# Optimization experiments

Hardware: AMD Instinct MI355X
Metric: run time of the kernel (lower is better)

Reference implementation:

```python
import jax, jax.numpy as jnp
import numpy as np

B, H, W = 8, 256, 256
C = 32          # out_channels / lifted width
CK = 4          # raw k-field channels
M1, M2 = 12, 12  # retained Fourier modes


def _dense_init(key, cin, cout):
    kw, _ = jax.random.split(key)
    w = jax.random.normal(kw, (cin, cout), jnp.float32) / np.float32(np.sqrt(cin))
    b = jnp.zeros((cout,), jnp.float32)
    return w, b


def setup_inputs() -> dict:
    key = jax.random.key(0)
    ks = jax.random.split(key, 16)
    d = {}
    d["x"] = jax.random.normal(ks[0], (B, H, W, C), jnp.float32)
    d["k"] = jax.random.normal(ks[1], (B, H, W, CK), jnp.float32)
    # Project L: Dense(CK->2C), Dense(2C->C)
    d["L_w1"], d["L_b1"] = _dense_init(ks[2], CK, 2 * C)
    d["L_w2"], d["L_b2"] = _dense_init(ks[3], 2 * C, C)
    # Project G
    d["G_w1"], d["G_b1"] = _dense_init(ks[4], CK, 2 * C)
    d["G_w2"], d["G_b2"] = _dense_init(ks[5], 2 * C, C)
    # plain Dense layers
    d["u_w"], d["u_b"] = _dense_init(ks[6], C, C)
    d["Wu_w"], d["Wu_b"] = _dense_init(ks[7], C, C)
    d["Hu_w"], d["Hu_b"] = _dense_init(ks[8], C, C)
    d["Ms_w"], d["Ms_b"] = _dense_init(ks[9], CK, C)
    d["out_w"], d["out_b"] = _dense_init(ks[10], C, C)
    # spectral kernels, init scale = 1/(C_in*C_out)
    scale = np.float32(1.0 / (C * C))
    d["k1r"] = scale * jax.random.normal(ks[11], (C, C, M1, M2), jnp.float32)
    d["k1i"] = scale * jax.random.normal(ks[12], (C, C, M1, M2), jnp.float32)
    d["k2r"] = scale * jax.random.normal(ks[13], (C, C, M1, M2), jnp.float32)
    d["k2i"] = scale * jax.random.normal(ks[14], (C, C, M1, M2), jnp.float32)
    return d


def _project(v, w1, b1, w2, b2):
    return jax.nn.gelu(v @ w1 + b1) @ w2 + b2


def _spectral_conv(v, k1r, k1i, k2r, k2i):
    # v: [B,H,W,C] -> rfft over (H,W); x_ft: [B,H,W//2+1,C] complex
    v_ft = jnp.fft.rfftn(v, axes=(1, 2))
    s1 = jnp.einsum('bijc,coij->bijo', v_ft[:, :M1, :M2, :], k1r + 1j * k1i)
    s2 = jnp.einsum('bijc,coij->bijo', v_ft[:, -M1:, :M2, :], k2r + 1j * k2i)
    out_ft = jnp.zeros_like(v_ft)
    out_ft = out_ft.at[:, :M1, :M2, :].set(s1)
    out_ft = out_ft.at[:, -M1:, :M2, :].set(s2)
    return jnp.fft.irfftn(out_ft, axes=(1, 2))


def reference(x, k,
              L_w1, L_b1, L_w2, L_b2,
              G_w1, G_b1, G_w2, G_b2,
              u_w, u_b, Wu_w, Wu_b, Hu_w, Hu_b, Ms_w, Ms_b,
              out_w, out_b,
              k1r, k1i, k2r, k2i):
    L = _project(k, L_w1, L_b1, L_w2, L_b2)   # [B,H,W,C]
    G = _project(k, G_w1, G_b1, G_w2, G_b2)   # [B,H,W,C]
    u = x @ u_w + u_b
    Wu = u @ Wu_w + Wu_b
    Hu = u @ Hu_w + Hu_b
    Ms = k @ Ms_w + Ms_b
    Fv = _spectral_conv(L * u + Ms, k1r, k1i, k2r, k2i)
    born = Wu - G * (Hu - Fv)
    return jax.nn.gelu(born @ out_w + out_b)
```

## Files before the change

### kernel.cpp

```cpp
#include <hip/hip_runtime.h>
#include <hip/hip_bf16.h>
#include <math.h>

#define BB 8
#define NMODE 24

typedef __attribute__((ext_vector_type(8))) short bf16x8;
typedef __attribute__((ext_vector_type(4))) short bf16x4;
typedef __attribute__((ext_vector_type(4))) float f32x4;

#define MFMA32(a,b,c) __builtin_amdgcn_mfma_f32_16x16x32_bf16(a,b,c,0,0,0)

#if __has_builtin(__builtin_amdgcn_mfma_f32_16x16x16bf16_1k)
#define MFMA16(a,b,c) __builtin_amdgcn_mfma_f32_16x16x16bf16_1k(a,b,c,0,0,0)
#else
static __device__ __forceinline__ f32x4 MFMA16(bf16x4 a, bf16x4 b, f32x4 c){
    f32x4 d;
    asm("v_mfma_f32_16x16x16_bf16 %0, %1, %2, %3" : "=v"(d) : "v"(a), "v"(b), "v"(c));
    return d;
}
#endif

__device__ __forceinline__ unsigned pk2(float lo, float hi){
    __hip_bfloat162 h = __float22bfloat162_rn(make_float2(lo, hi));
    unsigned u; __builtin_memcpy(&u, &h, 4);
    return u;
}
__device__ __forceinline__ short f2b(float f){
    unsigned u = pk2(f, f);
    return (short)u;
}
__device__ __forceinline__ float b2f(short s){
    unsigned u = ((unsigned)(unsigned short)s) << 16;
    return __builtin_bit_cast(float, u);
}
__device__ __forceinline__ bf16x4 cvt4(f32x4 v){
    uint2 t; t.x = pk2(v[0], v[1]); t.y = pk2(v[2], v[3]);
    return __builtin_bit_cast(bf16x4, t);
}
__device__ __forceinline__ bf16x8 cvt8(float4 a, float4 b){
    uint4 t; t.x = pk2(a.x, a.y); t.y = pk2(a.z, a.w);
    t.z = pk2(b.x, b.y); t.w = pk2(b.z, b.w);
    return __builtin_bit_cast(bf16x8, t);
}
__device__ __forceinline__ float gelu_f(float v) {
    float v2  = v * v;
    float arg = v * fmaf(0.10294294f, v2, 2.30220795f);
    float s   = __builtin_amdgcn_exp2f(arg);
    float rc  = __builtin_amdgcn_rcpf(1.0f + s);
    return v - v * rc;
}

__global__ __launch_bounds__(256) void kern0(
    const float* __restrict__ Lw1, const float* __restrict__ Lb1, const float* __restrict__ Lw2,
    const float* __restrict__ Gw1, const float* __restrict__ Gb1, const float* __restrict__ Gw2,
    const float* __restrict__ uw,
    const float* __restrict__ Wuw, const float* __restrict__ Huw,
    const float* __restrict__ Msw, const float* __restrict__ Msb,
    const float* __restrict__ ow,  const float* __restrict__ ob,
    const float* __restrict__ Wub,
    const float* __restrict__ k1r, const float* __restrict__ k1i,
    const float* __restrict__ k2r, const float* __restrict__ k2i,
    short* __restrict__ G1a, short* __restrict__ L1a,
    short* __restrict__ G2T, short* __restrict__ L2T,
    short* __restrict__ WuT, short* __restrict__ HuT,
    short* __restrict__ owT, short* __restrict__ uwT, short* __restrict__ MsA,
    short* __restrict__ basisW, short* __restrict__ basis2P,
    short* __restrict__ basisH1, short* __restrict__ basisH3,
    short* __restrict__ Kp, float* __restrict__ obP)
{
    const int bid = blockIdx.x, t = threadIdx.x;
    const float tp = 6.28318530717958648f/256.f;
    if (bid == 0){
        for (int idx=t; idx<1024; idx+=256){
            int o = idx>>5, c = idx&31;
            WuT[o*32+c] = f2b(Wuw[c*32+o]);
        }
    } else if (bid == 1){
        for (int idx=t; idx<1024; idx+=256){
            int o = idx>>5, c = idx&31;
            HuT[o*32+c] = f2b(Huw[c*32+o]);
        }
    } else if (bid == 2){
        for (int idx=t; idx<1024; idx+=256){
            int hd = idx>>4, k2 = idx&15;
            G1a[idx] = f2b(k2<4 ? Gw1[k2*64+hd] : (k2==4 ? Gb1[hd] : 0.f));
            L1a[idx] = f2b(k2<4 ? Lw1[k2*64+hd] : (k2==4 ? Lb1[hd] : 0.f));
        }
    } else if (bid == 3){
        for (int idx=t; idx<2048; idx+=256){ int o=idx>>6, m=idx&63; G2T[idx]=f2b(Gw2[m*32+o]); }
    } else if (bid == 4){
        for (int idx=t; idx<2048; idx+=256){ int o=idx>>6, m=idx&63; L2T[idx]=f2b(Lw2[m*32+o]); }
    } else if (bid == 5){
        for (int idx=t; idx<1024; idx+=256){
            int o=idx>>5, c=idx&31;
            owT[idx]=f2b(ow[c*32+o]);
            uwT[idx]=f2b(uw[c*32+o]);
        }
    } else if (bid == 6){
        for (int idx=t; idx<512; idx+=256){
            int o=idx>>4, k2=idx&15;
            MsA[idx]=f2b(k2<4 ? Msw[k2*32+o] : (k2==4 ? Msb[o] : 0.f));
        }
        if (t < 32){
            float s = ob[t];
            for (int c=0;c<32;c++) s += Wub[c]*ow[c*32+t];
            obP[t] = s;
        }
    } else if (bid < 15){
        int base=(bid-7)*1024;
        for (int i=t; i<1024; i+=256){
            int idx=base+i; int m=idx>>8, w=idx&255;
            float v=0.f;
            if (m<12)       v = cosf(tp*(float)((m*w)&255));
            else if (m<24)  v = sinf(tp*(float)(((m-12)*w)&255));
            basisW[idx]=f2b(v);
        }
    } else if (bid < 23){
        int base=(bid-15)*1024;
        for (int i=t; i<1024; i+=256){
            int idx=base+i; int w=idx>>5, k=idx&31;
            float v=0.f;
            if (k<24){ int m=k>>1; float a=tp*(float)((m*w)&255); v=(k&1)? -sinf(a):cosf(a); }
            basis2P[idx]=f2b(v);
        }
    } else if (bid < 27){
        int base=(bid-23)*3072;
        for (int i=t; i<3072; i+=256){
            int idx=base+i; int m = idx>>8, h = idx&255;
            int mm = m % 24;
            int ia = (mm<12) ? mm : 232+mm;
            float a = tp*(float)((ia*h)&255);
            basisH1[idx] = f2b(m<24 ? cosf(a) : sinf(a));
        }
    } else if (bid < 35){
        int base=(bid-27)*2048;
        for (int i=t; i<2048; i+=256){
            int idx=base+i; int h = idx>>6, k = idx&63;
            float v = 0.f;
            if (k < 48){
                int mm = k % 24;
                int ia = (mm<12) ? mm : 232+mm;
                float a = tp*(float)((ia*h)&255);
                v = (k<24) ? cosf(a) : sinf(a);
            }
            basisH3[idx] = f2b(v);
        }
    } else {
        int base=(bid-35)*8192;
        for (int i=t; i<8192; i+=256){
            int pid = base + i;
            int o = pid & 31, c = (pid>>5) & 31;
            int rest = pid >> 10;
            int ii = rest % 24, jj = rest / 24;
            int iis = (ii<12) ? ii : ii-12;
            const float* wr = (ii<12) ? k1r : k2r;
            const float* wi = (ii<12) ? k1i : k2i;
            size_t widx = ((size_t)(c*32 + o)*12 + iis)*12 + jj;
            float sc = (jj==0 ? 1.f : 2.f) / 65536.f;
            Kp[2*pid]   = f2b(wr[widx] * sc);
            Kp[2*pid+1] = f2b(wi[widx] * sc);
        }
    }
}


__global__ __launch_bounds__(256, 3) void kernAG(
    const float* __restrict__ x, const float* __restrict__ kk,
    const float* __restrict__ Lb2, const float* __restrict__ ubv,
    const float* __restrict__ Gb2,
    const short* __restrict__ L1a, const short* __restrict__ L2T,
    const short* __restrict__ G1a, const short* __restrict__ G2T,
    const short* __restrict__ uwT, const short* __restrict__ MsA,
    const short* __restrict__ basisW, float* __restrict__ A1,
    float* __restrict__ outw)
{
    __shared__ short vT[32*264];
    const int tid = threadIdx.x, l = tid&63, wv = tid>>6;
    const int q = l>>4, r = l&15;
    const f32x4 z4 = {0.f,0.f,0.f,0.f};

    if (blockIdx.x >= (unsigned)(BB*256)){
        const int bh = blockIdx.x - BB*256;
        short* ug = (short*)outw + (size_t)bh*16384;

        bf16x4 ga[4], g2f[2][4];
        #pragma unroll
        for (int mt=0; mt<4; mt++) ga[mt] = *(const bf16x4*)(G1a + (r+16*mt)*16 + 4*q);
        #pragma unroll
        for (int mt=0; mt<2; mt++)
            #pragma unroll
            for (int ks=0; ks<4; ks++)
                g2f[mt][ks] = *(const bf16x4*)(G2T + (r+16*mt)*64 + 16*ks + 4*q);
        f32x4 gb2v[2];
        #pragma unroll
        for (int mt=0; mt<2; mt++) gb2v[mt] = *(const f32x4*)(Gb2 + 16*mt + 4*q);

        bf16x4 kB[4];
        #pragma unroll
        for (int nt=0; nt<4; nt++){
            const int p = wv*64 + nt*16 + r;
            bf16x4 t = {0,0,0,0};
            if (q==0){
                float4 k4 = *(const float4*)(kk + ((size_t)bh*256 + p)*4);
                uint2 pkk; pkk.x = pk2(k4.x, k4.y); pkk.y = pk2(k4.z, k4.w);
                t = __builtin_bit_cast(bf16x4, pkk);
            } else if (q==1){ t[0] = (short)0x3F80; }
            kB[nt] = t;
        }

        bf16x4 hidG[4][4];
        #pragma unroll
        for (int nt=0; nt<4; nt++)
            #pragma unroll
            for (int mt=0; mt<4; mt++){
                f32x4 acc = MFMA16(ga[mt], kB[nt], z4);
                f32x4 g;
                #pragma unroll
                for (int i=0;i<4;i++) g[i]=gelu_f(acc[i]);
                hidG[nt][mt] = cvt4(g);
            }

        #pragma unroll
        for (int nt=0; nt<4; nt++){
            #pragma unroll
            for (int mt=0; mt<2; mt++){
                f32x4 aG  = MFMA16(g2f[mt][0], hidG[nt][0], gb2v[mt]);
                f32x4 aG2 = MFMA16(g2f[mt][1], hidG[nt][1], z4);
                aG  = MFMA16(g2f[mt][2], hidG[nt][2], aG);
                aG2 = MFMA16(g2f[mt][3], hidG[nt][3], aG2);
                f32x4 gs;
                #pragma unroll
                for (int rg=0; rg<4; rg++) gs[rg] = aG[rg] + aG2[rg];
                *(bf16x4*)(ug + (8 + nt*2+mt)*1024 + tid*4) = cvt4(gs);
            }
        }
        return;
    }

    const int bh = blockIdx.x, b = bh>>8, h = bh&255;

    bf16x4 la[4], ma[2], l2f[2][4];
    bf16x8 ua8[2];
    #pragma unroll
    for (int mt=0; mt<4; mt++) la[mt] = *(const bf16x4*)(L1a + (r+16*mt)*16 + 4*q);
    #pragma unroll
    for (int mt=0; mt<2; mt++){
        ma[mt]  = *(const bf16x4*)(MsA + (r+16*mt)*16 + 4*q);
        ua8[mt] = *(const bf16x8*)(uwT + (r+16*mt)*32 + 8*q);
        #pragma unroll
        for (int ks=0; ks<4; ks++)
            l2f[mt][ks] = *(const bf16x4*)(L2T + (r+16*mt)*64 + 16*ks + 4*q);
    }
    f32x4 lb2v[2], ubv4[2];
    #pragma unroll
    for (int mt=0; mt<2; mt++){
        lb2v[mt] = *(const f32x4*)(Lb2 + 16*mt + 4*q);
        ubv4[mt] = *(const f32x4*)(ubv + 16*mt + 4*q);
    }

    #pragma unroll
    for (int nt=0; nt<4; nt++){
        const int p = wv*64 + nt*16 + r;
        const float* xp = x + ((size_t)bh*256 + p)*32 + 8*q;
        float4 x0 = *(const float4*)xp;
        float4 x1 = *(const float4*)(xp + 4);
        bf16x8 xB8 = cvt8(x0, x1);
        bf16x4 kB = {0,0,0,0};
        if (q==0){
            float4 k4 = *(const float4*)(kk + ((size_t)bh*256 + p)*4);
            uint2 pkk; pkk.x = pk2(k4.x, k4.y); pkk.y = pk2(k4.z, k4.w);
            kB = __builtin_bit_cast(bf16x4, pkk);
        } else if (q==1){ kB[0] = (short)0x3F80; }

        bf16x4 hidL[4];
        #pragma unroll
        for (int mt=0; mt<4; mt++){
            f32x4 accL = MFMA16(la[mt], kB, z4);
            f32x4 gl;
            #pragma unroll
            for (int i=0;i<4;i++) gl[i]=gelu_f(accL[i]);
            hidL[mt] = cvt4(gl);
        }
        #pragma unroll
        for (int mt=0; mt<2; mt++){
            f32x4 aU = MFMA32(ua8[mt], xB8, ubv4[mt]);
            f32x4 aM = MFMA16(ma[mt], kB, z4);
            f32x4 aL  = MFMA16(l2f[mt][0], hidL[0], lb2v[mt]);
            f32x4 aL2 = MFMA16(l2f[mt][1], hidL[1], z4);
            aL  = MFMA16(l2f[mt][2], hidL[2], aL);
            aL2 = MFMA16(l2f[mt][3], hidL[3], aL2);
            f32x4 vv;
            #pragma unroll
            for (int rg=0; rg<4; rg++) vv[rg] = (aL[rg]+aL2[rg]) * aU[rg] + aM[rg];
            bf16x4 vb = cvt4(vv);
            #pragma unroll
            for (int rg=0; rg<4; rg++)
                vT[(16*mt + 4*q + rg)*264 + p] = vb[rg];
        }
    }
    __syncthreads();

    const int mt2 = wv>>1, nt2 = wv&1;
    f32x4 accD = z4;
    #pragma unroll
    for (int ks=0; ks<8; ks++){
        bf16x8 av = *(const bf16x8*)(basisW + (r+16*mt2)*256 + 32*ks + 8*q);
        bf16x8 bv = *(const bf16x8*)(&vT[(r+16*nt2)*264 + 32*ks + 8*q]);
        accD = MFMA32(av, bv, accD);
    }
    #pragma unroll
    for (int rg=0; rg<4; rg++){
        int mode = 16*mt2 + 4*q + rg;
        int ch = r + 16*nt2;
        if (mode < 12)
            A1[((size_t)(b*12+mode)*256 + h)*64 + ch*2] = accD[rg];
        else if (mode < 24)
            A1[((size_t)(b*12+mode-12)*256 + h)*64 + ch*2 + 1] = -accD[rg];
    }
}

__global__ __launch_bounds__(512) void kernC1(
    const float* __restrict__ A1, const short* __restrict__ basisH1,
    const short* __restrict__ Kp, short* __restrict__ SBg)
{
    __shared__ short AT[64*264];
    __shared__ float C1L[48*66];
    const int bj = blockIdx.x;
    const int j  = bj % 12;
    const int tid = threadIdx.x, l = tid&63;
    const int w = tid>>6;
    const int q = l>>4, r = l&15;
    const f32x4 z4 = {0.f,0.f,0.f,0.f};

    {
        const float* Ag = A1 + (size_t)bj*16384;
        for (int i = tid; i < 4096; i += 512){
            float4 v = *(const float4*)(Ag + i*4);
            int hh = (i*4) >> 6;
            int cc = (i*4) & 63;
            AT[(cc+0)*264 + hh] = f2b(v.x);
            AT[(cc+1)*264 + hh] = f2b(v.y);
            AT[(cc+2)*264 + hh] = f2b(v.z);
            AT[(cc+3)*264 + hh] = f2b(v.w);
        }
    }
    __syncthreads();

    {
        const int nt  = w & 3;
        const int nmt = (w < 4) ? 2 : 1;
        const int mt0 = (w < 4) ? 0 : 2;
        f32x4 acc[2] = {z4, z4};
        #pragma unroll
        for (int ks=0; ks<8; ks++){
            bf16x8 bv = *(const bf16x8*)(AT + (nt*16 + r)*264 + ks*32 + q*8);
            #pragma unroll
            for (int mi=0; mi<2; mi++){
                if (mi < nmt){
                    bf16x8 av = *(const bf16x8*)(basisH1 + (r + 16*(mt0+mi))*256 + ks*32 + q*8);
                    acc[mi] = MFMA32(av, bv, acc[mi]);
                }
            }
        }
        #pragma unroll
        for (int mi=0; mi<2; mi++){
            if (mi < nmt){
                #pragma unroll
                for (int rg=0; rg<4; rg++)
                    C1L[(16*(mt0+mi) + 4*q + rg)*66 + 16*nt + r] = acc[mi][rg];
            }
        }
    }
    __syncthreads();

    {
        const int o = tid & 31, g = tid >> 5;
        short* SB = SBg + (size_t)bj*4096;
        #pragma unroll
        for (int half=0; half<2; half++){
            int i = g + 16*half;
            if (i < 24){
                float Sre=0.f, Sim=0.f;
                const short* kp = Kp + ((size_t)(j*24 + i)*32)*64 + 2*o;
                #pragma unroll 4
                for (int c=0; c<32; c++){
                    float vr = C1L[i*66 + 2*c]     + C1L[(24+i)*66 + 2*c+1];
                    float vi = C1L[i*66 + 2*c + 1] - C1L[(24+i)*66 + 2*c];
                    short2 kv = *(const short2*)(kp + c*64);
                    float kr = b2f(kv.x), ki = b2f(kv.y);
                    Sre += vr*kr - vi*ki;
                    Sim += vr*ki + vi*kr;
                }
                SB[o*64 + i]           = f2b(Sre);
                SB[o*64 + 24 + i]      = f2b(-Sim);
                SB[2048 + o*64 + i]    = f2b(Sim);
                SB[2048 + o*64 + 24+i] = f2b(Sre);
            }
        }
        int o2 = (tid >> 4) & 31, kz = 48 + (tid & 15);
        SB[o2*64 + kz] = 0;
        SB[2048 + o2*64 + kz] = 0;
    }
}

__global__ __launch_bounds__(256) void kernC2(
    const short* __restrict__ basisH3, const short* __restrict__ SBg,
    const float* __restrict__ Hub, short* __restrict__ Tp)
{
    __shared__ __align__(16) short Tt[16*1024];
    const int bid = blockIdx.x;
    const int b = bid >> 4, ht = bid & 15;
    const int tid = threadIdx.x, l = tid&63, w = tid>>6;
    const int q = l>>4, r = l&15;
    const f32x4 z4 = {0.f,0.f,0.f,0.f};

    for (int idx = tid; idx < 512; idx += 256){
        int hh = idx >> 5, o = idx & 31;
        #pragma unroll
        for (int kkz=0; kkz<8; kkz++) Tt[(hh*32+o)*32 + 24 + kkz] = 0;
    }

    bf16x8 af[2];
    #pragma unroll
    for (int ks=0; ks<2; ks++)
        af[ks] = *(const bf16x8*)(basisH3 + (ht*16 + r)*64 + ks*32 + q*8);

    #pragma unroll
    for (int jj=0; jj<3; jj++){
        int j = w*3 + jj;
        const short* SB = SBg + (size_t)(b*12 + j)*4096;
        #pragma unroll
        for (int nt=0; nt<2; nt++){
            f32x4 aRe = z4, aIm = z4;
            #pragma unroll
            for (int ks=0; ks<2; ks++){
                bf16x8 b1 = *(const bf16x8*)(SB + (16*nt + r)*64 + ks*32 + q*8);
                bf16x8 b2 = *(const bf16x8*)(SB + 2048 + (16*nt + r)*64 + ks*32 + q*8);
                aRe = MFMA32(af[ks], b1, aRe);
                aIm = MFMA32(af[ks], b2, aIm);
            }
            if (j == 0){
                float hb = Hub[16*nt + r];
                #pragma unroll
                for (int rg=0; rg<4; rg++) aRe[rg] -= hb;
            }
            #pragma unroll
            for (int rg=0; rg<4; rg++){
                int hl = 4*q + rg, o = 16*nt + r;
                *(unsigned*)&Tt[(hl*32 + o)*32 + 2*j] = pk2(aRe[rg], aIm[rg]);
            }
        }
    }
    __syncthreads();

    short* dst = Tp + (size_t)(b*256 + ht*16)*1024;
    #pragma unroll
    for (int it=0; it<8; it++){
        int off = (tid + it*256)*8;
        *(int4*)(dst + off) = *(const int4*)&Tt[off];
    }
}

__global__ __launch_bounds__(256, 3) void kernD(
    const float* __restrict__ x, const float* __restrict__ ubv,
    const float* __restrict__ obP,
    const short* __restrict__ uwT,
    const short* __restrict__ WuT, const short* __restrict__ HuT,
    const short* __restrict__ owT, const short* __restrict__ basis2P,
    const short* __restrict__ Tp, float* out)
{
    const int bh = blockIdx.x;
    const int tid = threadIdx.x, l = tid&63, wv = tid>>6;
    const int q = l>>4, r = l&15;
    const f32x4 z4 = {0.f,0.f,0.f,0.f};
    const short* ug = (const short*)out + (size_t)bh*16384;

    bf16x4 Gf[4][2];
    bf16x8 bb8[4];
    float4 x0[4], x1[4];
    #pragma unroll
    for (int nt=0; nt<4; nt++){
        const int p = wv*64 + nt*16 + r;
        #pragma unroll
        for (int ks=0; ks<2; ks++)
            Gf[nt][ks] = *(const bf16x4*)(ug + (8 + nt*2+ks)*1024 + tid*4);
        bb8[nt] = *(const bf16x8*)(basis2P + p*32 + 8*q);
        const float* xp = x + ((size_t)bh*256 + p)*32 + 8*q;
        x0[nt] = *(const float4*)xp;
        x1[nt] = *(const float4*)(xp + 4);
    }
    bf16x8 tp8[2], ua8[2];
    bf16x4 wuf[2][2], huf[2][2], owf[2][2];
    f32x4 obv2[2], ubv4[2];
    #pragma unroll
    for (int mt=0; mt<2; mt++){
        tp8[mt] = *(const bf16x8*)(Tp + (size_t)bh*1024 + (r+16*mt)*32 + 8*q);
        ua8[mt] = *(const bf16x8*)(uwT + (r+16*mt)*32 + 8*q);
        #pragma unroll
        for (int ks=0; ks<2; ks++){
            wuf[mt][ks] = *(const bf16x4*)(WuT + (r+16*mt)*32 + 16*ks + 4*q);
            huf[mt][ks] = *(const bf16x4*)(HuT + (r+16*mt)*32 + 16*ks + 4*q);
            owf[mt][ks] = *(const bf16x4*)(owT + (r+16*mt)*32 + 16*ks + 4*q);
        }
        obv2[mt] = *(const f32x4*)(obP + 16*mt + 4*q);
        ubv4[mt] = *(const f32x4*)(ubv + 16*mt + 4*q);
    }
    __syncthreads();

    #pragma unroll
    for (int nt=0; nt<4; nt++){
        const int p = wv*64 + nt*16 + r;

        bf16x8 xB8 = cvt8(x0[nt], x1[nt]);
        bf16x4 uB[2];
        #pragma unroll
        for (int mt=0; mt<2; mt++)
            uB[mt] = cvt4(MFMA32(ua8[mt], xB8, ubv4[mt]));

        bf16x4 bornB[2];
        #pragma unroll
        for (int mt=0; mt<2; mt++){
            f32x4 aFv = MFMA32(tp8[mt], bb8[nt], z4);
            f32x4 aHu = MFMA16(huf[mt][0], uB[0], z4);
            aHu = MFMA16(huf[mt][1], uB[1], aHu);
            f32x4 aW  = MFMA16(wuf[mt][0], uB[0], z4);
            aW  = MFMA16(wuf[mt][1], uB[1], aW);
            f32x4 brn;
            #pragma unroll
            for (int rg=0; rg<4; rg++)
                brn[rg] = aW[rg] - b2f(Gf[nt][mt][rg]) * (aHu[rg] - aFv[rg]);
            bornB[mt] = cvt4(brn);
        }
        #pragma unroll
        for (int mt=0; mt<2; mt++){
            f32x4 aO = MFMA16(owf[mt][0], bornB[0], obv2[mt]);
            aO = MFMA16(owf[mt][1], bornB[1], aO);
            float4 res;
            res.x = gelu_f(aO[0]);
            res.y = gelu_f(aO[1]);
            res.z = gelu_f(aO[2]);
            res.w = gelu_f(aO[3]);
            *(float4*)(out + ((size_t)bh*256 + p)*32 + 16*mt + 4*q) = res;
        }
    }
}

extern "C" void kernel_launch(void* const* d_in, const int* in_sizes, int n_in,
                              void* d_out, int out_size, void* d_ws, size_t ws_size,
                              hipStream_t stream)
{
    const float* x   = (const float*)d_in[0];
    const float* kk  = (const float*)d_in[1];
    const float* Lw1 = (const float*)d_in[2];
    const float* Lb1 = (const float*)d_in[3];
    const float* Lw2 = (const float*)d_in[4];
    const float* Lb2 = (const float*)d_in[5];
    const float* Gw1 = (const float*)d_in[6];
    const float* Gb1 = (const float*)d_in[7];
    const float* Gw2 = (const float*)d_in[8];
    const float* Gb2 = (const float*)d_in[9];
    const float* uw  = (const float*)d_in[10];
    const float* ub  = (const float*)d_in[11];
    const float* Wuw = (const float*)d_in[12];
    const float* Wub = (const float*)d_in[13];
    const float* Huw = (const float*)d_in[14];
    const float* Hub = (const float*)d_in[15];
    const float* Msw = (const float*)d_in[16];
    const float* Msb = (const float*)d_in[17];
    const float* ow  = (const float*)d_in[18];
    const float* ob  = (const float*)d_in[19];
    const float* k1r = (const float*)d_in[20];
    const float* k1i = (const float*)d_in[21];
    const float* k2r = (const float*)d_in[22];
    const float* k2i = (const float*)d_in[23];

    float* A1 = (float*)d_ws;
    short* Tp = (short*)(A1 + 1572864);
    short* tab = Tp + 2097152;
    short* G1a  = tab;
    short* L1a  = G1a + 1024;
    short* G2T  = L1a + 1024;
    short* L2T  = G2T + 2048;
    short* WuT  = L2T + 2048;
    short* HuT  = WuT + 1024;
    short* owT  = HuT + 1024;
    short* uwT  = owT + 1024;
    short* MsA  = uwT + 1024;
    short* basisW  = MsA + 512;
    short* basis2P = basisW + 8192;
    short* basisH1 = basis2P + 8192;
    short* basisH3 = basisH1 + 12288;
    short* Kp   = basisH3 + 16384;
    short* SBg  = Kp + 589824;
    float* obP  = (float*)(SBg + 393216);

    float* outp = (float*)d_out;

    kern0<<<71, 256, 0, stream>>>(Lw1, Lb1, Lw2, Gw1, Gb1, Gw2, uw,
                                  Wuw, Huw, Msw, Msb, ow, ob, Wub,
                                  k1r, k1i, k2r, k2i,
                                  G1a, L1a, G2T, L2T, WuT, HuT, owT, uwT, MsA,
                                  basisW, basis2P, basisH1, basisH3, Kp, obP);
    kernAG<<<BB*256*2, 256, 0, stream>>>(x, kk, Lb2, ub, Gb2,
                                         L1a, L2T, G1a, G2T, uwT, MsA, basisW,
                                         A1, outp);
    kernC1<<<BB*12, 512, 0, stream>>>(A1, basisH1, Kp, SBg);
    kernC2<<<BB*16, 256, 0, stream>>>(basisH3, SBg, Hub, Tp);
    kernD<<<BB*256, 256, 0, stream>>>(x, ub, obP, uwT, WuT, HuT, owT,
                                      basis2P, Tp, outp);
}
```

Measured before the change: 124.5 us.

## Stash u in bf16 from kernAG and reuse in kernD instead of recomputing

kernAG now writes the lifted u activation as bf16 into the scratch area of the output buffer, next to the already stored G. kernD reads that u back instead of reloading the fp32 x input and recomputing u with MFMA, so it reads half as many bytes per pixel and drops the uwT/ubv operands. Launch bounds are raised (kernAG 8, kernD 6) to allow more waves per CU. The risk is more global writes in kernAG and register spills under the tighter launch bounds.

```diff
diff --git a/kernel.cpp b/kernel.cpp
--- a/kernel.cpp
+++ b/kernel.cpp
@@ -165,7 +165,7 @@
 }
 
 
-__global__ __launch_bounds__(256, 3) void kernAG(
+__global__ __launch_bounds__(256, 8) void kernAG(
     const float* __restrict__ x, const float* __restrict__ kk,
     const float* __restrict__ Lb2, const float* __restrict__ ubv,
     const float* __restrict__ Gb2,
@@ -239,6 +239,7 @@
     }
 
     const int bh = blockIdx.x, b = bh>>8, h = bh&255;
+    short* ug = (short*)outw + (size_t)bh*16384;
 
     bf16x4 la[4], ma[2], l2f[2][4];
     bf16x8 ua8[2];
@@ -285,6 +286,7 @@
         #pragma unroll
         for (int mt=0; mt<2; mt++){
             f32x4 aU = MFMA32(ua8[mt], xB8, ubv4[mt]);
+            *(bf16x4*)(ug + (nt*2+mt)*1024 + tid*4) = cvt4(aU);
             f32x4 aM = MFMA16(ma[mt], kB, z4);
             f32x4 aL  = MFMA16(l2f[mt][0], hidL[0], lb2v[mt]);
             f32x4 aL2 = MFMA16(l2f[mt][1], hidL[1], z4);
@@ -462,10 +464,8 @@
     }
 }
 
-__global__ __launch_bounds__(256, 3) void kernD(
-    const float* __restrict__ x, const float* __restrict__ ubv,
+__global__ __launch_bounds__(256, 6) void kernD(
     const float* __restrict__ obP,
-    const short* __restrict__ uwT,
     const short* __restrict__ WuT, const short* __restrict__ HuT,
     const short* __restrict__ owT, const short* __restrict__ basis2P,
     const short* __restrict__ Tp, float* out)
@@ -476,27 +476,24 @@
     const f32x4 z4 = {0.f,0.f,0.f,0.f};
     const short* ug = (const short*)out + (size_t)bh*16384;
 
-    bf16x4 Gf[4][2];
+    bf16x4 uB[4][2], Gf[4][2];
     bf16x8 bb8[4];
-    float4 x0[4], x1[4];
     #pragma unroll
     for (int nt=0; nt<4; nt++){
         const int p = wv*64 + nt*16 + r;
         #pragma unroll
-        for (int ks=0; ks<2; ks++)
+        for (int ks=0; ks<2; ks++){
+            uB[nt][ks] = *(const bf16x4*)(ug + (nt*2+ks)*1024 + tid*4);
             Gf[nt][ks] = *(const bf16x4*)(ug + (8 + nt*2+ks)*1024 + tid*4);
+        }
         bb8[nt] = *(const bf16x8*)(basis2P + p*32 + 8*q);
-        const float* xp = x + ((size_t)bh*256 + p)*32 + 8*q;
-        x0[nt] = *(const float4*)xp;
-        x1[nt] = *(const float4*)(xp + 4);
-    }
-    bf16x8 tp8[2], ua8[2];
+    }
+    bf16x8 tp8[2];
     bf16x4 wuf[2][2], huf[2][2], owf[2][2];
-    f32x4 obv2[2], ubv4[2];
+    f32x4 obv2[2];
     #pragma unroll
     for (int mt=0; mt<2; mt++){
         tp8[mt] = *(const bf16x8*)(Tp + (size_t)bh*1024 + (r+16*mt)*32 + 8*q);
-        ua8[mt] = *(const bf16x8*)(uwT + (r+16*mt)*32 + 8*q);
         #pragma unroll
         for (int ks=0; ks<2; ks++){
             wuf[mt][ks] = *(const bf16x4*)(WuT + (r+16*mt)*32 + 16*ks + 4*q);
@@ -504,28 +501,20 @@
             owf[mt][ks] = *(const bf16x4*)(owT + (r+16*mt)*32 + 16*ks + 4*q);
         }
         obv2[mt] = *(const f32x4*)(obP + 16*mt + 4*q);
-        ubv4[mt] = *(const f32x4*)(ubv + 16*mt + 4*q);
     }
     __syncthreads();
 
     #pragma unroll
     for (int nt=0; nt<4; nt++){
         const int p = wv*64 + nt*16 + r;
-
-        bf16x8 xB8 = cvt8(x0[nt], x1[nt]);
-        bf16x4 uB[2];
-        #pragma unroll
-        for (int mt=0; mt<2; mt++)
-            uB[mt] = cvt4(MFMA32(ua8[mt], xB8, ubv4[mt]));
-
         bf16x4 bornB[2];
         #pragma unroll
         for (int mt=0; mt<2; mt++){
             f32x4 aFv = MFMA32(tp8[mt], bb8[nt], z4);
-            f32x4 aHu = MFMA16(huf[mt][0], uB[0], z4);
-            aHu = MFMA16(huf[mt][1], uB[1], aHu);
-            f32x4 aW  = MFMA16(wuf[mt][0], uB[0], z4);
-            aW  = MFMA16(wuf[mt][1], uB[1], aW);
+            f32x4 aHu = MFMA16(huf[mt][0], uB[nt][0], z4);
+            aHu = MFMA16(huf[mt][1], uB[nt][1], aHu);
+            f32x4 aW  = MFMA16(wuf[mt][0], uB[nt][0], z4);
+            aW  = MFMA16(wuf[mt][1], uB[nt][1], aW);
             f32x4 brn;
             #pragma unroll
             for (int rg=0; rg<4; rg++)
@@ -607,6 +596,5 @@
                                          A1, outp);
     kernC1<<<BB*12, 512, 0, stream>>>(A1, basisH1, Kp, SBg);
     kernC2<<<BB*16, 256, 0, stream>>>(basisH3, SBg, Hub, Tp);
-    kernD<<<BB*256, 256, 0, stream>>>(x, ub, obP, uwT, WuT, HuT, owT,
-                                      basis2P, Tp, outp);
-}
+    kernD<<<BB*256, 256, 0, stream>>>(obP, WuT, HuT, owT, basis2P, Tp, outp);
+}
```

Measured after the change: 169.1 us. +35.8%, slower.
